# Optimization experiments

Hardware: AMD Instinct MI355X
Metric: run time of the kernel (lower is better)

## Reference

```python
import jax, jax.numpy as jnp
import numpy as np

B, S, D = 4, 4096, 2048
DQ = D // 4          # router hidden
DF = 4 * D           # layer_fn FFN hidden
CAPACITY = 0.125


def setup_inputs() -> dict:
    key = jax.random.key(0)
    ks = jax.random.split(key, 5)
    sc = 0.02
    return {
        "x":   jax.random.normal(ks[0], (B, S, D), jnp.float32),
        "Wr1": jax.random.normal(ks[1], (D, DQ), jnp.float32) * sc,
        "br1": jnp.zeros((DQ,), jnp.float32),
        "Wr2": jax.random.normal(ks[2], (DQ, 1), jnp.float32) * sc,
        "br2": jnp.zeros((1,), jnp.float32),
        "Wf1": jax.random.normal(ks[3], (D, DF), jnp.float32) * sc,
        "bf1": jnp.zeros((DF,), jnp.float32),
        "Wf2": jax.random.normal(ks[4], (DF, D), jnp.float32) * sc,
        "bf2": jnp.zeros((D,), jnp.float32),
    }


def reference(x, Wr1, br1, Wr2, br2, Wf1, bf1, Wf2, bf2):
    b, s, d = x.shape
    k = max(1, int(CAPACITY * s))

    # router: Linear -> ReLU -> Linear -> squeeze(-1)
    h = jax.nn.relu(jnp.einsum("bsd,dq->bsq", x, Wr1) + br1)
    scores = (jnp.einsum("bsq,qo->bso", h, Wr2) + br2)[..., 0]   # [B, S]

    # top-k token selection per batch row
    topk_scores, topk_idx = jax.lax.top_k(scores, k)             # [B, k]

    # gather selected tokens
    sel = jnp.take_along_axis(x, topk_idx[..., None], axis=1)    # [B, k, D]

    # layer_fn: standard FFN (D -> 4D -> D) on selected tokens only
    proc = jnp.einsum("bkf,fd->bkd",
                      jax.nn.relu(jnp.einsum("bkd,df->bkf", sel, Wf1) + bf1),
                      Wf2) + bf2                                 # [B, k, D]

    # scatter processed tokens back into a copy of x
    batch_idx = jnp.arange(b)[:, None]                           # [B, 1]
    output = x.at[batch_idx, topk_idx].set(proc)                 # [B, S, D]

    mask = jnp.zeros((b, s), dtype=bool).at[batch_idx, topk_idx].set(True)
    return output, mask
```

## Files before the change

kernel.cpp:

```cpp
#include <hip/hip_runtime.h>

#define B_    4
#define S_    4096
#define D_    2048
#define DQ_   512
#define DF_   8192
#define KSEL_ 512
#define M_    (B_ * S_)
#define MS_   (B_ * KSEL_)

typedef __attribute__((ext_vector_type(8))) short bf16x8;
typedef __attribute__((ext_vector_type(4))) float f32x4;
typedef __attribute__((address_space(3))) void as3_void;
typedef const __attribute__((address_space(1))) void as1_cvoid;

__device__ __forceinline__ unsigned short f2bf(float f) {
    unsigned u = __float_as_uint(f);
    u += 0x7FFFu + ((u >> 16) & 1u);
    return (unsigned short)(u >> 16);
}
__device__ __forceinline__ float bf2f(unsigned short h) {
    return __uint_as_float(((unsigned)h) << 16);
}

__device__ __forceinline__ void gload16(const void* g, void* l) {
    __builtin_amdgcn_global_load_lds((as1_cvoid*)g, (as3_void*)l, 16, 0, 0);
}

__global__ void split_copy_kernel(const float* __restrict__ x,
                                  unsigned short* __restrict__ xh,
                                  unsigned short* __restrict__ xl,
                                  float* __restrict__ out, int n8) {
    int i = blockIdx.x * blockDim.x + threadIdx.x;
    int stride = gridDim.x * blockDim.x;
    for (; i < n8; i += stride) {
        float4 a = ((const float4*)x)[2 * i];
        float4 b = ((const float4*)x)[2 * i + 1];
        ((float4*)out)[2 * i]     = a;
        ((float4*)out)[2 * i + 1] = b;
        float v[8] = {a.x, a.y, a.z, a.w, b.x, b.y, b.z, b.w};
        unsigned short hi[8], lo[8];
#pragma unroll
        for (int j = 0; j < 8; j++) {
            hi[j] = f2bf(v[j]);
            lo[j] = f2bf(v[j] - bf2f(hi[j]));
        }
        *(uint4*)(xh + (size_t)i * 8) = *(const uint4*)hi;
        *(uint4*)(xl + (size_t)i * 8) = *(const uint4*)lo;
    }
}

__global__ void wsplit_kernel(const float* __restrict__ W,
                              unsigned short* __restrict__ whiT,
                              unsigned short* __restrict__ wloT) {
    __shared__ float tile[32][33];
    int tx = threadIdx.x, ty = threadIdx.y;
    int n0 = blockIdx.x * 32, k0 = blockIdx.y * 32;
#pragma unroll
    for (int j = 0; j < 4; j++)
        tile[ty + j * 8][tx] = W[(size_t)(k0 + ty + j * 8) * DQ_ + n0 + tx];
    __syncthreads();
#pragma unroll
    for (int j = 0; j < 4; j++) {
        float v = tile[tx][ty + j * 8];
        unsigned short hi = f2bf(v);
        unsigned short lo = f2bf(v - bf2f(hi));
        size_t row = (size_t)(n0 + ty + j * 8) * D_;
        whiT[row + k0 + tx] = hi;
        wloT[row + k0 + tx] = lo;
    }
}

__global__ void transpose_bf16_kernel(const float* __restrict__ in,
                                      unsigned short* __restrict__ out,
                                      int R, int C) {
    __shared__ float tile[32][33];
    int tx = threadIdx.x, ty = threadIdx.y;
    int c0 = blockIdx.x * 32, r0 = blockIdx.y * 32;
#pragma unroll
    for (int j = 0; j < 4; j++)
        tile[ty + j * 8][tx] = in[(size_t)(r0 + ty + j * 8) * C + c0 + tx];
    __syncthreads();
#pragma unroll
    for (int j = 0; j < 4; j++)
        out[(size_t)(c0 + ty + j * 8) * R + r0 + tx] = f2bf(tile[tx][ty + j * 8]);
}

#define RSTAGE(bufp, ktX) do {                                              \
    const size_t ko_ = (size_t)(ktX) * 32;                                  \
    char* laH_ = (char*)(&sA[bufp][0][0]) + w * 1024;                       \
    char* laL_ = (char*)(&sA[bufp][1][0]) + w * 1024;                       \
    char* lbH_ = (char*)(&sB[bufp][0][0]) + w * 1024;                       \
    char* lbL_ = (char*)(&sB[bufp][1][0]) + w * 1024;                       \
    gload16(gAh + ko_,            laH_);                                    \
    gload16(gAh + 64 * D_ + ko_,  laH_ + 4096);                             \
    gload16(gAl + ko_,            laL_);                                    \
    gload16(gAl + 64 * D_ + ko_,  laL_ + 4096);                             \
    gload16(gBh + ko_,            lbH_);                                    \
    gload16(gBh + 64 * D_ + ko_,  lbH_ + 4096);                             \
    gload16(gBl + ko_,            lbL_);                                    \
    gload16(gBl + 64 * D_ + ko_,  lbL_ + 4096);                             \
  } while (0)

__global__ __launch_bounds__(256) void router_mfma(const unsigned short* __restrict__ xh,
                                                   const unsigned short* __restrict__ xl,
                                                   const unsigned short* __restrict__ whiT,
                                                   const unsigned short* __restrict__ wloT,
                                                   const float* __restrict__ br1,
                                                   const float* __restrict__ Wr2,
                                                   float* __restrict__ pscore) {
    __shared__ unsigned short sA[2][2][128 * 32];
    __shared__ unsigned short sB[2][2][128 * 32];
    const int t = threadIdx.x;
    const int w = t >> 6, l = t & 63;
    const int m0 = blockIdx.x * 128, n0 = blockIdx.y * 128;
    const int wr = w >> 1, wc = w & 1;

    f32x4 acc[4][4];
    const f32x4 zz = {0.f, 0.f, 0.f, 0.f};
#pragma unroll
    for (int m = 0; m < 4; m++)
#pragma unroll
        for (int n = 0; n < 4; n++) acc[m][n] = zz;

    const int srow = t >> 2;
    const int sch8 = (((t & 3) ^ ((t >> 3) & 3)) * 8);
    const unsigned short* gAh = xh + (size_t)(m0 + srow) * D_ + sch8;
    const unsigned short* gAl = xl + (size_t)(m0 + srow) * D_ + sch8;
    const unsigned short* gBh = whiT + (size_t)(n0 + srow) * D_ + sch8;
    const unsigned short* gBl = wloT + (size_t)(n0 + srow) * D_ + sch8;

    RSTAGE(0, 0);
    RSTAGE(1, 1);

    const int fro = ((l >> 4) ^ ((l >> 1) & 3)) * 8;
    const int arB = (wr * 64 + (l & 15)) * 32 + fro;
    const int brB = (wc * 64 + (l & 15)) * 32 + fro;

    for (int kt = 0; kt < 64; ++kt) {
        if (kt + 1 < 64) { asm volatile("s_waitcnt vmcnt(8)" ::: "memory"); }
        else             { asm volatile("s_waitcnt vmcnt(0)" ::: "memory"); }
        __builtin_amdgcn_s_barrier();
        __builtin_amdgcn_sched_barrier(0);
        const int cur = kt & 1;
        const unsigned short* LAh = &sA[cur][0][0];
        const unsigned short* LAl = &sA[cur][1][0];
        const unsigned short* LBh = &sB[cur][0][0];
        const unsigned short* LBl = &sB[cur][1][0];
        bf16x8 ah[4], al[4], bh[4], bl[4];
#pragma unroll
        for (int f = 0; f < 4; f++) ah[f] = *(const bf16x8*)(LAh + arB + f * 512);
#pragma unroll
        for (int f = 0; f < 4; f++) bh[f] = *(const bf16x8*)(LBh + brB + f * 512);
#pragma unroll
        for (int f = 0; f < 4; f++) bl[f] = *(const bf16x8*)(LBl + brB + f * 512);
#pragma unroll
        for (int f = 0; f < 4; f++) al[f] = *(const bf16x8*)(LAl + arB + f * 512);
        __builtin_amdgcn_s_setprio(1);
#pragma unroll
        for (int m = 0; m < 4; m++)
#pragma unroll
            for (int n = 0; n < 4; n++)
                acc[m][n] = __builtin_amdgcn_mfma_f32_16x16x32_bf16(ah[m], bh[n], acc[m][n], 0, 0, 0);
#pragma unroll
        for (int m = 0; m < 4; m++)
#pragma unroll
            for (int n = 0; n < 4; n++)
                acc[m][n] = __builtin_amdgcn_mfma_f32_16x16x32_bf16(ah[m], bl[n], acc[m][n], 0, 0, 0);
#pragma unroll
        for (int m = 0; m < 4; m++)
#pragma unroll
            for (int n = 0; n < 4; n++)
                acc[m][n] = __builtin_amdgcn_mfma_f32_16x16x32_bf16(al[m], bh[n], acc[m][n], 0, 0, 0);
        __builtin_amdgcn_s_setprio(0);
        __builtin_amdgcn_sched_barrier(0);
        __builtin_amdgcn_s_barrier();
        if (kt + 2 < 64) RSTAGE(cur, kt + 2);
    }

    float br1v[4], wr2v[4];
#pragma unroll
    for (int nf = 0; nf < 4; nf++) {
        int col = n0 + wc * 64 + nf * 16 + (l & 15);
        br1v[nf] = br1[col];
        wr2v[nf] = Wr2[col];
    }
#pragma unroll
    for (int mf = 0; mf < 4; mf++)
#pragma unroll
        for (int q = 0; q < 4; q++) {
            float s = 0.f;
#pragma unroll
            for (int nf = 0; nf < 4; nf++)
                s += fmaxf(acc[mf][nf][q] + br1v[nf], 0.f) * wr2v[nf];
#pragma unroll
            for (int off = 8; off >= 1; off >>= 1)
                s += __shfl_xor(s, off);
            if ((l & 15) == 0) {
                int row = m0 + wr * 64 + mf * 16 + (l >> 4) * 4 + q;
                pscore[(size_t)(blockIdx.y * 2 + wc) * M_ + row] = s;
            }
        }
}

__global__ __launch_bounds__(1024) void topk_kernel(const float* __restrict__ pscore,
                                                    const float* __restrict__ br2,
                                                    int* __restrict__ sel_idx,
                                                    float* __restrict__ maskF) {
    __shared__ unsigned hist[4096];
    __shared__ unsigned long long cand[4096];
    __shared__ unsigned char flags[S_];
    __shared__ unsigned cnts[2];
    __shared__ unsigned s_thr, s_above;
    int b = blockIdx.x, t = threadIdx.x;
    float bb = br2[0];

    for (int i = t; i < 4096; i += 1024) { hist[i] = 0; flags[i] = 0; }
    if (t < 2) cnts[t] = 0;
    __syncthreads();

    unsigned ureg[4];
#pragma unroll
    for (int r = 0; r < 4; r++) {
        int i = t + r * 1024;
        float f = bb;
#pragma unroll
        for (int s8 = 0; s8 < 8; s8++) f += pscore[(size_t)s8 * M_ + b * S_ + i];
        unsigned u = __float_as_uint(f);
        u = (u & 0x80000000u) ? ~u : (u | 0x80000000u);
        ureg[r] = u;
        atomicAdd(&hist[u >> 20], 1u);
    }
    __syncthreads();

    for (int d = 1; d < 4096; d <<= 1) {
        unsigned tmp[4];
#pragma unroll
        for (int r = 0; r < 4; r++) {
            int i = t + r * 1024;
            tmp[r] = (i + d < 4096) ? hist[i + d] : 0u;
        }
        __syncthreads();
#pragma unroll
        for (int r = 0; r < 4; r++) hist[t + r * 1024] += tmp[r];
        __syncthreads();
    }
#pragma unroll
    for (int r = 0; r < 4; r++) {
        int i = t + r * 1024;
        unsigned Si = hist[i];
        unsigned Sn = (i + 1 < 4096) ? hist[i + 1] : 0u;
        if (Si >= KSEL_ && Sn < KSEL_) { s_thr = (unsigned)i; s_above = Sn; }
    }
    __syncthreads();
    const unsigned thr = s_thr;
    const unsigned need = KSEL_ - s_above;

#pragma unroll
    for (int r = 0; r < 4; r++) {
        int i = t + r * 1024;
        unsigned u = ureg[r];
        unsigned bin = u >> 20;
        if (bin > thr) flags[i] = 1;
        else if (bin == thr) {
            unsigned slot = atomicAdd(&cnts[0], 1u);
            cand[slot] = ((unsigned long long)u << 32) | (unsigned)(S_ - 1 - i);
        }
    }
    __syncthreads();

    unsigned nc = cnts[0];
    unsigned ncp2 = 1; while (ncp2 < nc) ncp2 <<= 1;
    for (unsigned i = t + nc; i < ncp2; i += 1024) cand[i] = 0ull;
    __syncthreads();
    for (unsigned k = 2; k <= ncp2; k <<= 1)
        for (unsigned j = k >> 1; j > 0; j >>= 1) {
            for (unsigned i = t; i < ncp2; i += 1024) {
                unsigned li = i ^ j;
                if (li > i) {
                    unsigned long long a = cand[i], c = cand[li];
                    bool up = ((i & k) == 0);
                    if (up ? (a > c) : (a < c)) { cand[i] = c; cand[li] = a; }
                }
            }
            __syncthreads();
        }
    for (unsigned i = t; i < need; i += 1024) {
        unsigned long long kk = cand[ncp2 - need + i];
        flags[(S_ - 1) - (int)(kk & 0xFFFFFFFFu)] = 1;
    }
    __syncthreads();

#pragma unroll
    for (int r = 0; r < 4; r++) {
        int i = t + r * 1024;
        if (flags[i]) {
            unsigned slot = atomicAdd(&cnts[1], 1u);
            sel_idx[b * KSEL_ + slot] = i;
        }
        maskF[b * S_ + i] = flags[i] ? 1.0f : 0.0f;
    }
}

__global__ void gather_kernel(const float* __restrict__ x, const int* __restrict__ sel_idx,
                              unsigned short* __restrict__ sel) {
    int jrow = blockIdx.x;
    int b = jrow >> 9;
    int tok = sel_idx[jrow];
    const float* src = x + ((size_t)(b * S_ + tok)) * D_;
    int t = threadIdx.x;
    float4 v0 = ((const float4*)src)[2 * t];
    float4 v1 = ((const float4*)src)[2 * t + 1];
    unsigned p0 = (unsigned)f2bf(v0.x) | ((unsigned)f2bf(v0.y) << 16);
    unsigned p1 = (unsigned)f2bf(v0.z) | ((unsigned)f2bf(v0.w) << 16);
    unsigned p2 = (unsigned)f2bf(v1.x) | ((unsigned)f2bf(v1.y) << 16);
    unsigned p3 = (unsigned)f2bf(v1.z) | ((unsigned)f2bf(v1.w) << 16);
    *(uint4*)(sel + (size_t)jrow * D_ + t * 8) = make_uint4(p0, p1, p2, p3);
}

#define STAGEAB(bufp, ktX) do {                                                   \
    const unsigned short* a_ = gA + (size_t)(ktX) * 64;                           \
    const unsigned short* b_ = gB + (size_t)(ktX) * 64;                           \
    char* la_ = (char*)(&lds[bufp][0][0]) + w * 1024;                             \
    char* lb_ = (char*)(&lds[bufp][1][0]) + w * 1024;                             \
    gload16(a_,                      la_);                                        \
    gload16(a_ +  64 * (size_t)K,    la_ + 8192);                                 \
    gload16(a_ + 128 * (size_t)K,    la_ + 16384);                                \
    gload16(a_ + 192 * (size_t)K,    la_ + 24576);                                \
    gload16(b_,                      lb_);                                        \
    gload16(b_ +  64 * (size_t)K,    lb_ + 8192);                                 \
    gload16(b_ + 128 * (size_t)K,    lb_ + 16384);                                \
    gload16(b_ + 192 * (size_t)K,    lb_ + 24576);                                \
  } while (0)

__global__ __launch_bounds__(512) void mfma_gemm256(const unsigned short* __restrict__ A,
                                                    const unsigned short* __restrict__ Bt,
                                                    int M, int N, int K, int kspan,
                                                    const float* __restrict__ bias,
                                                    unsigned short* __restrict__ Cbf,
                                                    unsigned short* __restrict__ partialB,
                                                    int epi) {
    __shared__ unsigned short lds[2][2][256 * 64];
    const int t = threadIdx.x;
    const int w = t >> 6, l = t & 63;
    const int m0 = blockIdx.y * 256, n0 = blockIdx.x * 256;
    const int wr = w >> 2, wc = w & 3;
    const int kbeg = blockIdx.z * kspan;
    const int NT = kspan / 64;

    f32x4 acc[8][4];
    const f32x4 zz = {0.f, 0.f, 0.f, 0.f};
#pragma unroll
    for (int m = 0; m < 8; m++)
#pragma unroll
        for (int n = 0; n < 4; n++) acc[m][n] = zz;

    const int srow = t >> 3;
    const int sch8 = (((t & 7) ^ ((t >> 3) & 7)) * 8);
    const unsigned short* gA = A + (size_t)(m0 + srow) * K + kbeg + sch8;
    const unsigned short* gB = Bt + (size_t)(n0 + srow) * K + kbeg + sch8;

    STAGEAB(0, 0);
    STAGEAB(1, 1);

    for (int kt = 0; kt < NT; ++kt) {
        if (kt + 1 < NT) { asm volatile("s_waitcnt vmcnt(8)" ::: "memory"); }
        else             { asm volatile("s_waitcnt vmcnt(0)" ::: "memory"); }
        __builtin_amdgcn_s_barrier();
        __builtin_amdgcn_sched_barrier(0);
        const int cur = kt & 1;
        const unsigned short* LA = &lds[cur][0][0];
        const unsigned short* LB = &lds[cur][1][0];
#pragma unroll
        for (int kk = 0; kk < 2; kk++) {
            const int sw_ = ((kk * 4 + (l >> 4)) ^ (l & 7)) * 8;
            bf16x8 bfr[4], af0[4], af1[4];
#pragma unroll
            for (int n = 0; n < 4; n++)
                bfr[n] = *(const bf16x8*)(LB + (wc * 64 + n * 16 + (l & 15)) * 64 + sw_);
#pragma unroll
            for (int m = 0; m < 4; m++) {
                af0[m] = *(const bf16x8*)(LA + (wr * 128 + m * 16 + (l & 15)) * 64 + sw_);
                af1[m] = *(const bf16x8*)(LA + (wr * 128 + 64 + m * 16 + (l & 15)) * 64 + sw_);
            }
            __builtin_amdgcn_s_setprio(1);
#pragma unroll
            for (int m = 0; m < 4; m++)
#pragma unroll
                for (int n = 0; n < 4; n++)
                    acc[m][n] = __builtin_amdgcn_mfma_f32_16x16x32_bf16(af0[m], bfr[n], acc[m][n], 0, 0, 0);
#pragma unroll
            for (int m = 0; m < 4; m++)
#pragma unroll
                for (int n = 0; n < 4; n++)
                    acc[4 + m][n] = __builtin_amdgcn_mfma_f32_16x16x32_bf16(af1[m], bfr[n], acc[4 + m][n], 0, 0, 0);
            __builtin_amdgcn_s_setprio(0);
        }
        __builtin_amdgcn_sched_barrier(0);
        __builtin_amdgcn_s_barrier();
        if (kt + 2 < NT) STAGEAB(cur, kt + 2);
    }

    if (epi == 0) {
#pragma unroll
        for (int m = 0; m < 8; m++) {
            int rowb = m0 + wr * 128 + m * 16 + (l >> 4) * 4;
#pragma unroll
            for (int n = 0; n < 4; n++) {
                int col = n0 + wc * 64 + n * 16 + (l & 15);
                float bv = bias[col];
#pragma unroll
                for (int q = 0; q < 4; q++) {
                    float v = fmaxf(acc[m][n][q] + bv, 0.f);
                    Cbf[(size_t)(rowb + q) * N + col] = f2bf(v);
                }
            }
        }
    } else {
        unsigned short* pseg = partialB + (size_t)blockIdx.z * M * N;
#pragma unroll
        for (int m = 0; m < 8; m++) {
            int rowb = m0 + wr * 128 + m * 16 + (l >> 4) * 4;
#pragma unroll
            for (int n = 0; n < 4; n++) {
                int col = n0 + wc * 64 + n * 16 + (l & 15);
#pragma unroll
                for (int q = 0; q < 4; q++)
                    pseg[(size_t)(rowb + q) * N + col] = f2bf(acc[m][n][q]);
            }
        }
    }
}

__global__ void reduce_scatter_kernel(const unsigned short* __restrict__ partial,
                                      const float* __restrict__ bias,
                                      const int* __restrict__ sel_idx,
                                      float* __restrict__ out) {
    int m = blockIdx.x;
    int t = threadIdx.x;
    int brow = m >> 9;
    int tok = sel_idx[m];
    float* orow = out + ((size_t)(brow * S_ + tok)) * D_;
    int c = t * 8;
    const size_t seg = (size_t)MS_ * D_;
    const unsigned short* pb = partial + (size_t)m * D_ + c;
    float o[8];
#pragma unroll
    for (int j = 0; j < 8; j++) o[j] = bias[c + j];
#pragma unroll
    for (int s = 0; s < 4; s++) {
        uint4 v = *(const uint4*)(pb + s * seg);
        const unsigned short* e = (const unsigned short*)&v;
#pragma unroll
        for (int j = 0; j < 8; j++) o[j] += bf2f(e[j]);
    }
    *(float4*)(orow + c)     = *(float4*)&o[0];
    *(float4*)(orow + c + 4) = *(float4*)&o[4];
}

extern "C" void kernel_launch(void* const* d_in, const int* in_sizes, int n_in,
                              void* d_out, int out_size, void* d_ws, size_t ws_size,
                              hipStream_t stream) {
    const float* x   = (const float*)d_in[0];
    const float* Wr1 = (const float*)d_in[1];
    const float* br1 = (const float*)d_in[2];
    const float* Wr2 = (const float*)d_in[3];
    const float* br2 = (const float*)d_in[4];
    const float* Wf1 = (const float*)d_in[5];
    const float* bf1 = (const float*)d_in[6];
    const float* Wf2 = (const float*)d_in[7];
    const float* bf2 = (const float*)d_in[8];
    float* out = (float*)d_out;
    char* ws = (char*)d_ws;

    unsigned short* xh    = (unsigned short*)(ws);
    unsigned short* xl    = (unsigned short*)(ws + (64u << 20));
    unsigned short* whiT  = (unsigned short*)(ws + (160u << 20));
    unsigned short* wloT  = (unsigned short*)(ws + (162u << 20));
    float* pscore         = (float*)(ws + (168u << 20));
    int* sel_idx          = (int*)(ws + (169u << 20));
    unsigned short* partB = (unsigned short*)(ws);
    unsigned short* w1t   = (unsigned short*)(ws + (64u << 20));
    unsigned short* w2t   = (unsigned short*)(ws + (96u << 20));
    unsigned short* h1    = (unsigned short*)(ws + (128u << 20));
    unsigned short* sel   = (unsigned short*)(ws + (160u << 20));
    float* maskF          = out + (size_t)B_ * S_ * D_;

    (void)in_sizes; (void)n_in; (void)out_size; (void)ws_size;

    split_copy_kernel<<<2048, 256, 0, stream>>>(x, xh, xl, out, (M_ * D_) / 8);
    wsplit_kernel<<<dim3(DQ_ / 32, D_ / 32), dim3(32, 8), 0, stream>>>(Wr1, whiT, wloT);
    router_mfma<<<dim3(M_ / 128, DQ_ / 128), 256, 0, stream>>>(
        xh, xl, whiT, wloT, br1, Wr2, pscore);
    topk_kernel<<<B_, 1024, 0, stream>>>(pscore, br2, sel_idx, maskF);
    gather_kernel<<<MS_, 256, 0, stream>>>(x, sel_idx, sel);
    transpose_bf16_kernel<<<dim3(DF_ / 32, D_ / 32), dim3(32, 8), 0, stream>>>(Wf1, w1t, D_, DF_);
    transpose_bf16_kernel<<<dim3(D_ / 32, DF_ / 32), dim3(32, 8), 0, stream>>>(Wf2, w2t, DF_, D_);
    mfma_gemm256<<<dim3(DF_ / 256, MS_ / 256, 1), 512, 0, stream>>>(
        sel, w1t, MS_, DF_, D_, D_, bf1, h1, nullptr, 0);
    mfma_gemm256<<<dim3(D_ / 256, MS_ / 256, 4), 512, 0, stream>>>(
        h1, w2t, MS_, D_, DF_, DF_ / 4, nullptr, nullptr, partB, 1);
    reduce_scatter_kernel<<<MS_, 256, 0, stream>>>(partB, bf2, sel_idx, out);
}
```

Before: 386.1 us.

## Score router in single bf16 pass, refine only near-threshold candidates with 3-pass

The router GEMM over all tokens now uses only the high bf16 part (one MFMA pass instead of three). Tokens whose coarse score falls within a fixed band around the top-k threshold are gathered and rescored with the full hi/lo split-K 3-pass GEMM, and the final top-k is chosen from those refined scores. This targets the roughly threefold MFMA cost of the full-precision router. In exchange it adds several small kernels, and it relies on a fixed error band and a candidate cap of 384, which could give wrong selections if the coarse scores miss by more than the band or if too many tokens land near the threshold.

```diff
diff --git a/kernel.cpp b/kernel.cpp
--- a/kernel.cpp
+++ b/kernel.cpp
@@ -8,6 +8,9 @@
 #define KSEL_ 512
 #define M_    (B_ * S_)
 #define MS_   (B_ * KSEL_)
+#define CCAP_ 384
+#define CM_   (4 * CCAP_)
+#define RBAND 5.0e-3f
 
 typedef __attribute__((ext_vector_type(8))) short bf16x8;
 typedef __attribute__((ext_vector_type(4))) float f32x4;
@@ -21,6 +24,14 @@
 }
 __device__ __forceinline__ float bf2f(unsigned short h) {
     return __uint_as_float(((unsigned)h) << 16);
+}
+__device__ __forceinline__ unsigned ordu(float f) {
+    unsigned u = __float_as_uint(f);
+    return (u & 0x80000000u) ? ~u : (u | 0x80000000u);
+}
+__device__ __forceinline__ float inv_ordu(unsigned u) {
+    unsigned bits = (u & 0x80000000u) ? (u & 0x7FFFFFFFu) : ~u;
+    return __uint_as_float(bits);
 }
 
 __device__ __forceinline__ void gload16(const void* g, void* l) {
@@ -102,19 +113,194 @@
     gload16(gBl + 64 * D_ + ko_,  lbL_ + 4096);                             \
   } while (0)
 
-__global__ __launch_bounds__(256) void router_mfma(const unsigned short* __restrict__ xh,
-                                                   const unsigned short* __restrict__ xl,
-                                                   const unsigned short* __restrict__ whiT,
-                                                   const unsigned short* __restrict__ wloT,
-                                                   const float* __restrict__ br1,
-                                                   const float* __restrict__ Wr2,
-                                                   float* __restrict__ pscore) {
+#define RSTAGE_HI(bufp, ktX) do {                                           \
+    const size_t ko_ = (size_t)(ktX) * 32;                                  \
+    char* la_ = (char*)(&sA[bufp][0]) + w * 1024;                           \
+    char* lb_ = (char*)(&sB[bufp][0]) + w * 1024;                           \
+    gload16(gAh + ko_,            la_);                                     \
+    gload16(gAh + 64 * D_ + ko_,  la_ + 4096);                              \
+    gload16(gBh + ko_,            lb_);                                     \
+    gload16(gBh + 64 * D_ + ko_,  lb_ + 4096);                              \
+  } while (0)
+
+__global__ __launch_bounds__(256) void router_hi(const unsigned short* __restrict__ xh,
+                                                 const unsigned short* __restrict__ whiT,
+                                                 const float* __restrict__ br1,
+                                                 const float* __restrict__ Wr2,
+                                                 float* __restrict__ pscore) {
+    __shared__ unsigned short sA[2][128 * 32];
+    __shared__ unsigned short sB[2][128 * 32];
+    const int t = threadIdx.x;
+    const int w = t >> 6, l = t & 63;
+    const int m0 = blockIdx.x * 128, n0 = blockIdx.y * 128;
+    const int wr = w >> 1, wc = w & 1;
+
+    f32x4 acc[4][4];
+    const f32x4 zz = {0.f, 0.f, 0.f, 0.f};
+#pragma unroll
+    for (int m = 0; m < 4; m++)
+#pragma unroll
+        for (int n = 0; n < 4; n++) acc[m][n] = zz;
+
+    const int srow = t >> 2;
+    const int sch8 = (((t & 3) ^ ((t >> 3) & 3)) * 8);
+    const unsigned short* gAh = xh + (size_t)(m0 + srow) * D_ + sch8;
+    const unsigned short* gBh = whiT + (size_t)(n0 + srow) * D_ + sch8;
+
+    RSTAGE_HI(0, 0);
+    RSTAGE_HI(1, 1);
+
+    const int fro = ((l >> 4) ^ ((l >> 1) & 3)) * 8;
+    const int arB = (wr * 64 + (l & 15)) * 32 + fro;
+    const int brB = (wc * 64 + (l & 15)) * 32 + fro;
+
+    for (int kt = 0; kt < 64; ++kt) {
+        if (kt + 1 < 64) { asm volatile("s_waitcnt vmcnt(4)" ::: "memory"); }
+        else             { asm volatile("s_waitcnt vmcnt(0)" ::: "memory"); }
+        __builtin_amdgcn_s_barrier();
+        __builtin_amdgcn_sched_barrier(0);
+        const int cur = kt & 1;
+        const unsigned short* LA = &sA[cur][0];
+        const unsigned short* LB = &sB[cur][0];
+        bf16x8 ah[4], bh[4];
+#pragma unroll
+        for (int f = 0; f < 4; f++) ah[f] = *(const bf16x8*)(LA + arB + f * 512);
+#pragma unroll
+        for (int f = 0; f < 4; f++) bh[f] = *(const bf16x8*)(LB + brB + f * 512);
+        __builtin_amdgcn_s_setprio(1);
+#pragma unroll
+        for (int m = 0; m < 4; m++)
+#pragma unroll
+            for (int n = 0; n < 4; n++)
+                acc[m][n] = __builtin_amdgcn_mfma_f32_16x16x32_bf16(ah[m], bh[n], acc[m][n], 0, 0, 0);
+        __builtin_amdgcn_s_setprio(0);
+        __builtin_amdgcn_sched_barrier(0);
+        __builtin_amdgcn_s_barrier();
+        if (kt + 2 < 64) RSTAGE_HI(cur, kt + 2);
+    }
+
+    float br1v[4], wr2v[4];
+#pragma unroll
+    for (int nf = 0; nf < 4; nf++) {
+        int col = n0 + wc * 64 + nf * 16 + (l & 15);
+        br1v[nf] = br1[col];
+        wr2v[nf] = Wr2[col];
+    }
+#pragma unroll
+    for (int mf = 0; mf < 4; mf++)
+#pragma unroll
+        for (int q = 0; q < 4; q++) {
+            float s = 0.f;
+#pragma unroll
+            for (int nf = 0; nf < 4; nf++)
+                s += fmaxf(acc[mf][nf][q] + br1v[nf], 0.f) * wr2v[nf];
+#pragma unroll
+            for (int off = 8; off >= 1; off >>= 1)
+                s += __shfl_xor(s, off);
+            if ((l & 15) == 0) {
+                int row = m0 + wr * 64 + mf * 16 + (l >> 4) * 4 + q;
+                pscore[(size_t)(blockIdx.y * 2 + wc) * M_ + row] = s;
+            }
+        }
+}
+
+__global__ __launch_bounds__(1024) void topk_classify(const float* __restrict__ pscore,
+                                                      const float* __restrict__ br2,
+                                                      unsigned char* __restrict__ defs,
+                                                      int* __restrict__ cand_idx,
+                                                      int* __restrict__ cand_cnt,
+                                                      int* __restrict__ ndef) {
+    __shared__ unsigned hist[4096];
+    __shared__ unsigned s_thr;
+    int b = blockIdx.x, t = threadIdx.x;
+    float bb = br2[0];
+
+    for (int i = t; i < 4096; i += 1024) hist[i] = 0;
+    if (t == 0) { cand_cnt[b] = 0; ndef[b] = 0; }
+    __syncthreads();
+
+    float sreg[4];
+#pragma unroll
+    for (int r = 0; r < 4; r++) {
+        int i = t + r * 1024;
+        float f = bb;
+#pragma unroll
+        for (int s8 = 0; s8 < 8; s8++) f += pscore[(size_t)s8 * M_ + b * S_ + i];
+        sreg[r] = f;
+        atomicAdd(&hist[ordu(f) >> 20], 1u);
+    }
+    __syncthreads();
+
+    for (int d = 1; d < 4096; d <<= 1) {
+        unsigned tmp[4];
+#pragma unroll
+        for (int r = 0; r < 4; r++) {
+            int i = t + r * 1024;
+            tmp[r] = (i + d < 4096) ? hist[i + d] : 0u;
+        }
+        __syncthreads();
+#pragma unroll
+        for (int r = 0; r < 4; r++) hist[t + r * 1024] += tmp[r];
+        __syncthreads();
+    }
+#pragma unroll
+    for (int r = 0; r < 4; r++) {
+        int i = t + r * 1024;
+        unsigned Si = hist[i];
+        unsigned Sn = (i + 1 < 4096) ? hist[i + 1] : 0u;
+        if (Si >= KSEL_ && Sn < KSEL_) s_thr = (unsigned)i;
+    }
+    __syncthreads();
+    const unsigned T = s_thr;
+    const float c_hi = inv_ordu((T << 20) | 0xFFFFFu) + 2.0f * RBAND;
+    const float c_lo = inv_ordu(T << 20) - 2.0f * RBAND;
+
+#pragma unroll
+    for (int r = 0; r < 4; r++) {
+        int i = t + r * 1024;
+        float s = sreg[r];
+        unsigned char d = 0;
+        if (s > c_hi) { d = 1; atomicAdd(&ndef[b], 1); }
+        else if (s >= c_lo) {
+            int slot = atomicAdd(&cand_cnt[b], 1);
+            if (slot < CCAP_) cand_idx[b * CCAP_ + slot] = i;
+        }
+        defs[b * S_ + i] = d;
+    }
+}
+
+__global__ void cand_gather(const unsigned short* __restrict__ xh,
+                            const unsigned short* __restrict__ xl,
+                            const int* __restrict__ cand_idx,
+                            const int* __restrict__ cand_cnt,
+                            unsigned short* __restrict__ cH,
+                            unsigned short* __restrict__ cL) {
+    int j = blockIdx.x, b = blockIdx.y, t = threadIdx.x;
+    size_t drow = ((size_t)b * CCAP_ + j) * D_;
+    if (j < cand_cnt[b]) {
+        int tok = cand_idx[b * CCAP_ + j];
+        size_t srw = ((size_t)(b * S_ + tok)) * D_;
+        *(uint4*)(cH + drow + t * 8) = *(const uint4*)(xh + srw + t * 8);
+        *(uint4*)(cL + drow + t * 8) = *(const uint4*)(xl + srw + t * 8);
+    } else {
+        uint4 z = make_uint4(0, 0, 0, 0);
+        *(uint4*)(cH + drow + t * 8) = z;
+        *(uint4*)(cL + drow + t * 8) = z;
+    }
+}
+
+__global__ __launch_bounds__(256) void cand_gemm3(const unsigned short* __restrict__ cH,
+                                                  const unsigned short* __restrict__ cL,
+                                                  const unsigned short* __restrict__ whiT,
+                                                  const unsigned short* __restrict__ wloT,
+                                                  float* __restrict__ part) {
     __shared__ unsigned short sA[2][2][128 * 32];
     __shared__ unsigned short sB[2][2][128 * 32];
     const int t = threadIdx.x;
     const int w = t >> 6, l = t & 63;
     const int m0 = blockIdx.x * 128, n0 = blockIdx.y * 128;
     const int wr = w >> 1, wc = w & 1;
+    const int kbeg = blockIdx.z * 128;
 
     f32x4 acc[4][4];
     const f32x4 zz = {0.f, 0.f, 0.f, 0.f};
@@ -125,10 +311,10 @@
 
     const int srow = t >> 2;
     const int sch8 = (((t & 3) ^ ((t >> 3) & 3)) * 8);
-    const unsigned short* gAh = xh + (size_t)(m0 + srow) * D_ + sch8;
-    const unsigned short* gAl = xl + (size_t)(m0 + srow) * D_ + sch8;
-    const unsigned short* gBh = whiT + (size_t)(n0 + srow) * D_ + sch8;
-    const unsigned short* gBl = wloT + (size_t)(n0 + srow) * D_ + sch8;
+    const unsigned short* gAh = cH + (size_t)(m0 + srow) * D_ + kbeg + sch8;
+    const unsigned short* gAl = cL + (size_t)(m0 + srow) * D_ + kbeg + sch8;
+    const unsigned short* gBh = whiT + (size_t)(n0 + srow) * D_ + kbeg + sch8;
+    const unsigned short* gBl = wloT + (size_t)(n0 + srow) * D_ + kbeg + sch8;
 
     RSTAGE(0, 0);
     RSTAGE(1, 1);
@@ -137,9 +323,9 @@
     const int arB = (wr * 64 + (l & 15)) * 32 + fro;
     const int brB = (wc * 64 + (l & 15)) * 32 + fro;
 
-    for (int kt = 0; kt < 64; ++kt) {
-        if (kt + 1 < 64) { asm volatile("s_waitcnt vmcnt(8)" ::: "memory"); }
-        else             { asm volatile("s_waitcnt vmcnt(0)" ::: "memory"); }
+    for (int kt = 0; kt < 4; ++kt) {
+        if (kt + 1 < 4) { asm volatile("s_waitcnt vmcnt(8)" ::: "memory"); }
+        else            { asm volatile("s_waitcnt vmcnt(0)" ::: "memory"); }
         __builtin_amdgcn_s_barrier();
         __builtin_amdgcn_sched_barrier(0);
         const int cur = kt & 1;
@@ -175,130 +361,94 @@
         __builtin_amdgcn_s_setprio(0);
         __builtin_amdgcn_sched_barrier(0);
         __builtin_amdgcn_s_barrier();
-        if (kt + 2 < 64) RSTAGE(cur, kt + 2);
-    }
-
-    float br1v[4], wr2v[4];
-#pragma unroll
-    for (int nf = 0; nf < 4; nf++) {
-        int col = n0 + wc * 64 + nf * 16 + (l & 15);
-        br1v[nf] = br1[col];
-        wr2v[nf] = Wr2[col];
-    }
-#pragma unroll
-    for (int mf = 0; mf < 4; mf++)
-#pragma unroll
-        for (int q = 0; q < 4; q++) {
-            float s = 0.f;
-#pragma unroll
-            for (int nf = 0; nf < 4; nf++)
-                s += fmaxf(acc[mf][nf][q] + br1v[nf], 0.f) * wr2v[nf];
-#pragma unroll
-            for (int off = 8; off >= 1; off >>= 1)
-                s += __shfl_xor(s, off);
-            if ((l & 15) == 0) {
-                int row = m0 + wr * 64 + mf * 16 + (l >> 4) * 4 + q;
-                pscore[(size_t)(blockIdx.y * 2 + wc) * M_ + row] = s;
-            }
-        }
-}
-
-__global__ __launch_bounds__(1024) void topk_kernel(const float* __restrict__ pscore,
-                                                    const float* __restrict__ br2,
+        if (kt + 2 < 4) RSTAGE(cur, kt + 2);
+    }
+
+    float* pseg = part + (size_t)blockIdx.z * CM_ * DQ_;
+#pragma unroll
+    for (int mf = 0; mf < 4; mf++) {
+        int rb = m0 + wr * 64 + mf * 16 + (l >> 4) * 4;
+#pragma unroll
+        for (int nf = 0; nf < 4; nf++) {
+            int col = n0 + wc * 64 + nf * 16 + (l & 15);
+#pragma unroll
+            for (int q = 0; q < 4; q++)
+                pseg[(size_t)(rb + q) * DQ_ + col] = acc[mf][nf][q];
+        }
+    }
+}
+
+__global__ void cand_reduce(const float* __restrict__ part,
+                            const float* __restrict__ br1,
+                            const float* __restrict__ Wr2,
+                            const float* __restrict__ br2,
+                            float* __restrict__ cscore) {
+    __shared__ float wsum[4];
+    int r = blockIdx.x, t = threadIdx.x;
+    int c = t * 2;
+    float h0 = br1[c], h1 = br1[c + 1];
+#pragma unroll
+    for (int s = 0; s < 16; s++) {
+        const float* p = part + (size_t)s * CM_ * DQ_ + (size_t)r * DQ_ + c;
+        h0 += p[0];
+        h1 += p[1];
+    }
+    float s = fmaxf(h0, 0.f) * Wr2[c] + fmaxf(h1, 0.f) * Wr2[c + 1];
+#pragma unroll
+    for (int off = 32; off >= 1; off >>= 1) s += __shfl_xor(s, off);
+    if ((t & 63) == 0) wsum[t >> 6] = s;
+    __syncthreads();
+    if (t == 0) cscore[r] = wsum[0] + wsum[1] + wsum[2] + wsum[3] + br2[0];
+}
+
+__global__ __launch_bounds__(256) void final_select(const float* __restrict__ cscore,
+                                                    const int* __restrict__ cand_idx,
+                                                    const int* __restrict__ cand_cnt,
+                                                    const int* __restrict__ ndef,
+                                                    unsigned char* __restrict__ defs,
                                                     int* __restrict__ sel_idx,
                                                     float* __restrict__ maskF) {
-    __shared__ unsigned hist[4096];
-    __shared__ unsigned long long cand[4096];
-    __shared__ unsigned char flags[S_];
-    __shared__ unsigned cnts[2];
-    __shared__ unsigned s_thr, s_above;
+    __shared__ unsigned long long keys[512];
+    __shared__ unsigned slotc;
     int b = blockIdx.x, t = threadIdx.x;
-    float bb = br2[0];
-
-    for (int i = t; i < 4096; i += 1024) { hist[i] = 0; flags[i] = 0; }
-    if (t < 2) cnts[t] = 0;
-    __syncthreads();
-
-    unsigned ureg[4];
-#pragma unroll
-    for (int r = 0; r < 4; r++) {
-        int i = t + r * 1024;
-        float f = bb;
-#pragma unroll
-        for (int s8 = 0; s8 < 8; s8++) f += pscore[(size_t)s8 * M_ + b * S_ + i];
-        unsigned u = __float_as_uint(f);
-        u = (u & 0x80000000u) ? ~u : (u | 0x80000000u);
-        ureg[r] = u;
-        atomicAdd(&hist[u >> 20], 1u);
-    }
-    __syncthreads();
-
-    for (int d = 1; d < 4096; d <<= 1) {
-        unsigned tmp[4];
-#pragma unroll
-        for (int r = 0; r < 4; r++) {
-            int i = t + r * 1024;
-            tmp[r] = (i + d < 4096) ? hist[i + d] : 0u;
-        }
-        __syncthreads();
-#pragma unroll
-        for (int r = 0; r < 4; r++) hist[t + r * 1024] += tmp[r];
-        __syncthreads();
-    }
-#pragma unroll
-    for (int r = 0; r < 4; r++) {
-        int i = t + r * 1024;
-        unsigned Si = hist[i];
-        unsigned Sn = (i + 1 < 4096) ? hist[i + 1] : 0u;
-        if (Si >= KSEL_ && Sn < KSEL_) { s_thr = (unsigned)i; s_above = Sn; }
-    }
-    __syncthreads();
-    const unsigned thr = s_thr;
-    const unsigned need = KSEL_ - s_above;
-
-#pragma unroll
-    for (int r = 0; r < 4; r++) {
-        int i = t + r * 1024;
-        unsigned u = ureg[r];
-        unsigned bin = u >> 20;
-        if (bin > thr) flags[i] = 1;
-        else if (bin == thr) {
-            unsigned slot = atomicAdd(&cnts[0], 1u);
-            cand[slot] = ((unsigned long long)u << 32) | (unsigned)(S_ - 1 - i);
-        }
-    }
-    __syncthreads();
-
-    unsigned nc = cnts[0];
-    unsigned ncp2 = 1; while (ncp2 < nc) ncp2 <<= 1;
-    for (unsigned i = t + nc; i < ncp2; i += 1024) cand[i] = 0ull;
-    __syncthreads();
-    for (unsigned k = 2; k <= ncp2; k <<= 1)
-        for (unsigned j = k >> 1; j > 0; j >>= 1) {
-            for (unsigned i = t; i < ncp2; i += 1024) {
-                unsigned li = i ^ j;
+    int cnt = cand_cnt[b]; if (cnt > CCAP_) cnt = CCAP_;
+    int need = KSEL_ - ndef[b]; if (need > cnt) need = cnt; if (need < 0) need = 0;
+    if (t == 0) slotc = 0;
+
+    for (int i = t; i < 512; i += 256) {
+        unsigned long long k = 0ull;
+        if (i < cnt) {
+            int tok = cand_idx[b * CCAP_ + i];
+            unsigned u = ordu(cscore[b * CCAP_ + i]);
+            k = ((unsigned long long)u << 32) | (unsigned)(S_ - 1 - tok);
+        }
+        keys[i] = k;
+    }
+    __syncthreads();
+    for (int k = 2; k <= 512; k <<= 1)
+        for (int j = k >> 1; j > 0; j >>= 1) {
+            for (int i = t; i < 512; i += 256) {
+                int li = i ^ j;
                 if (li > i) {
-                    unsigned long long a = cand[i], c = cand[li];
+                    unsigned long long a = keys[i], c = keys[li];
                     bool up = ((i & k) == 0);
-                    if (up ? (a > c) : (a < c)) { cand[i] = c; cand[li] = a; }
+                    if (up ? (a > c) : (a < c)) { keys[i] = c; keys[li] = a; }
                 }
             }
             __syncthreads();
         }
-    for (unsigned i = t; i < need; i += 1024) {
-        unsigned long long kk = cand[ncp2 - need + i];
-        flags[(S_ - 1) - (int)(kk & 0xFFFFFFFFu)] = 1;
-    }
-    __syncthreads();
-
-#pragma unroll
-    for (int r = 0; r < 4; r++) {
-        int i = t + r * 1024;
-        if (flags[i]) {
-            unsigned slot = atomicAdd(&cnts[1], 1u);
+    for (int i = t; i < need; i += 256) {
+        unsigned long long kk = keys[512 - need + i];
+        int tok = (S_ - 1) - (int)(kk & 0xFFFFFFFFu);
+        defs[b * S_ + tok] = 1;
+    }
+    __syncthreads();
+    for (int i = t; i < S_; i += 256) {
+        if (defs[b * S_ + i]) {
+            unsigned slot = atomicAdd(&slotc, 1u);
             sel_idx[b * KSEL_ + slot] = i;
         }
-        maskF[b * S_ + i] = flags[i] ? 1.0f : 0.0f;
+        maskF[b * S_ + i] = defs[b * S_ + i] ? 1.0f : 0.0f;
     }
 }
 
@@ -475,9 +625,18 @@
 
     unsigned short* xh    = (unsigned short*)(ws);
     unsigned short* xl    = (unsigned short*)(ws + (64u << 20));
-    unsigned short* whiT  = (unsigned short*)(ws + (160u << 20));
-    unsigned short* wloT  = (unsigned short*)(ws + (162u << 20));
-    float* pscore         = (float*)(ws + (168u << 20));
+    unsigned short* whiT  = (unsigned short*)(ws + (128u << 20));
+    unsigned short* wloT  = (unsigned short*)(ws + (130u << 20));
+    float* pscore         = (float*)(ws + (132u << 20));
+    unsigned short* candH = (unsigned short*)(ws + (136u << 20));
+    unsigned short* candL = (unsigned short*)(ws + (144u << 20));
+    float* candPart       = (float*)(ws + (152u << 20));
+    candPart              = (float*)(ws + (170u << 20));
+    unsigned char* defs   = (unsigned char*)(ws + (168u << 20));
+    int* cand_idx         = (int*)(ws + (168u << 20) + 16384);
+    int* cand_cnt         = (int*)(ws + (168u << 20) + 24576);
+    int* ndef             = (int*)(ws + (168u << 20) + 24640);
+    float* cscore         = (float*)(ws + (168u << 20) + 32768);
     int* sel_idx          = (int*)(ws + (169u << 20));
     unsigned short* partB = (unsigned short*)(ws);
     unsigned short* w1t   = (unsigned short*)(ws + (64u << 20));
@@ -490,9 +649,12 @@
 
     split_copy_kernel<<<2048, 256, 0, stream>>>(x, xh, xl, out, (M_ * D_) / 8);
     wsplit_kernel<<<dim3(DQ_ / 32, D_ / 32), dim3(32, 8), 0, stream>>>(Wr1, whiT, wloT);
-    router_mfma<<<dim3(M_ / 128, DQ_ / 128), 256, 0, stream>>>(
-        xh, xl, whiT, wloT, br1, Wr2, pscore);
-    topk_kernel<<<B_, 1024, 0, stream>>>(pscore, br2, sel_idx, maskF);
+    router_hi<<<dim3(M_ / 128, DQ_ / 128), 256, 0, stream>>>(xh, whiT, br1, Wr2, pscore);
+    topk_classify<<<B_, 1024, 0, stream>>>(pscore, br2, defs, cand_idx, cand_cnt, ndef);
+    cand_gather<<<dim3(CCAP_, B_), 256, 0, stream>>>(xh, xl, cand_idx, cand_cnt, candH, candL);
+    cand_gemm3<<<dim3(CM_ / 128, DQ_ / 128, 16), 256, 0, stream>>>(candH, candL, whiT, wloT, candPart);
+    cand_reduce<<<CM_, 256, 0, stream>>>(candPart, br1, Wr2, br2, cscore);
+    final_select<<<B_, 256, 0, stream>>>(cscore, cand_idx, cand_cnt, ndef, defs, sel_idx, maskF);
     gather_kernel<<<MS_, 256, 0, stream>>>(x, sel_idx, sel);
     transpose_bf16_kernel<<<dim3(DF_ / 32, D_ / 32), dim3(32, 8), 0, stream>>>(Wf1, w1t, D_, DF_);
     transpose_bf16_kernel<<<dim3(D_ / 32, DF_ / 32), dim3(32, 8), 0, stream>>>(Wf2, w2t, DF_, D_);
```

Result: slower. 405.6 us (+5.0%).
